# Optimization experiments

Hardware: AMD Instinct MI355X
Metric: run time of the kernel (lower is better)

## Reference

```python
import jax, jax.numpy as jnp
import numpy as np

N, H, B = 1048576, 128, 4096


def setup_inputs() -> dict:
    key = jax.random.key(0)
    ks = jax.random.split(key, 10)
    x = jax.random.normal(ks[0], (N, H), dtype=jnp.float32)
    # sorted segment ids with every segment nonempty (matches torch.bincount/split usage)
    batch = jnp.sort(jnp.concatenate([
        jnp.arange(B, dtype=jnp.int32),
        jax.random.randint(ks[1], (N - B,), 0, B, dtype=jnp.int32),
    ]))
    s = 1.0 / np.sqrt(H)
    u = lambda k, shp: jax.random.uniform(k, shp, jnp.float32, -s, s)
    return {
        'session_embedding': x,
        'batch': batch,
        'W1': u(ks[2], (H, H)), 'b1': u(ks[3], (H,)),
        'W2': u(ks[4], (H, H)), 'b2': u(ks[5], (H,)),
        'Wq': u(ks[6], (1, H)), 'bq': u(ks[7], (1,)),
        'W3': u(ks[8], (H, 2 * H)), 'b3': u(ks[9], (H,)),
    }


def reference(session_embedding, batch, W1, b1, W2, b2, Wq, bq, W3, b3):
    # index of the last node in each session (batch is sorted)
    last_idx = jax.ops.segment_max(jnp.arange(N, dtype=jnp.int32), batch, num_segments=B)  # [B]
    v_n = session_embedding[last_idx]                      # [B, H]
    v_n_rep = v_n[batch]                                   # [N, H] last-node broadcast per node
    # attention logits: q(sigmoid(W1 v_n + W2 v_i))
    gate = jax.nn.sigmoid(v_n_rep @ W1.T + b1 + session_embedding @ W2.T + b2)  # [N, H]
    alpha = gate @ Wq.T + bq                               # [N, 1]
    s_g = jax.ops.segment_sum(alpha * session_embedding, batch, num_segments=B)  # [B, H]
    s_h = jnp.concatenate([v_n, s_g], axis=1) @ W3.T + b3  # [B, H]
    return s_h
```

## Files before the change

kernel.cpp:

```cpp
#include <hip/hip_runtime.h>
#include <hip/hip_bf16.h>

#define N_NODES 1048576
#define H 128
#define B_SESS 4096
#define TILE 64

typedef __attribute__((ext_vector_type(8))) short bf16x8;
typedef __attribute__((ext_vector_type(4))) short bf16x4;
typedef __attribute__((ext_vector_type(4))) float f32x4;

__device__ inline short bc(float f) {
  return (short)__builtin_bit_cast(unsigned short, __float2bfloat16(f));
}

__global__ void k_prep(const int* __restrict__ batch, int* __restrict__ last_idx,
                       const float* __restrict__ W2, unsigned short* __restrict__ W2b,
                       float* __restrict__ s_g) {
  int i = blockIdx.x * 256 + threadIdx.x;
  if (i < N_NODES) {
    if (i == N_NODES - 1 || batch[i] != batch[i + 1]) last_idx[batch[i]] = i;
  }
  if (i < B_SESS * H) s_g[i] = 0.f;
  if (i < 4096) {
    float4 v = *reinterpret_cast<const float4*>(W2 + (size_t)i * 4);
    bf16x4 o;
    o[0] = bc(v.x); o[1] = bc(v.y); o[2] = bc(v.z); o[3] = bc(v.w);
    *reinterpret_cast<bf16x4*>(W2b + (size_t)i * 4) = o;
  }
}

__global__ void k_apre(const float* __restrict__ x, const int* __restrict__ last_idx,
                       const float* __restrict__ W1, const float* __restrict__ b1,
                       const float* __restrict__ b2, float* __restrict__ A_pre) {
  __shared__ float Wl[128][132];
  __shared__ float vn[8][128];
  int t = threadIdx.x;
  for (int i = 0; i < 16; ++i) {
    int e = (t + i * 256) * 4;
    int r = e >> 7, c = e & 127;
    float4 v = *reinterpret_cast<const float4*>(W1 + e);
    Wl[r][c] = v.x; Wl[r][c + 1] = v.y; Wl[r][c + 2] = v.z; Wl[r][c + 3] = v.w;
  }
  int b0 = blockIdx.x * 8;
  for (int i = t; i < 8 * 128; i += 256) {
    int s = i >> 7, c = i & 127;
    vn[s][c] = x[(size_t)last_idx[b0 + s] * H + c];
  }
  __syncthreads();
  int h = t & 127, si = t >> 7;
  float bias = b1[h] + b2[h];
  for (int s = si; s < 8; s += 2) {
    float acc = bias;
    #pragma unroll
    for (int k = 0; k < 128; k += 4) {
      float4 w = *reinterpret_cast<const float4*>(&Wl[h][k]);
      acc += vn[s][k] * w.x + vn[s][k + 1] * w.y + vn[s][k + 2] * w.z + vn[s][k + 3] * w.w;
    }
    A_pre[(size_t)(b0 + s) * H + h] = acc;
  }
}

__global__ __launch_bounds__(256, 4)
void k_main(const float* __restrict__ x, const int* __restrict__ batch,
            const unsigned short* __restrict__ W2b, const float* __restrict__ Wq,
            const float* __restrict__ bq, const float* __restrict__ A_pre,
            float* __restrict__ s_g) {
  __shared__ unsigned short Wl[128][136];
  __shared__ float alph[TILE];
  __shared__ int bseg[TILE + 1];
  int t = threadIdx.x;
  int node0 = blockIdx.x * TILE;
  int w = t >> 6, lane = t & 63, r = lane & 15, ks = lane >> 4;
  int myrow = w * 16 + r;

  float4 af[8];
  const float* xrow = x + (size_t)(node0 + myrow) * H;
  #pragma unroll
  for (int k = 0; k < 4; ++k) {
    af[2 * k]     = *reinterpret_cast<const float4*>(xrow + k * 32 + ks * 8);
    af[2 * k + 1] = *reinterpret_cast<const float4*>(xrow + k * 32 + ks * 8 + 4);
  }
  #pragma unroll
  for (int i = 0; i < 8; ++i) {
    int e = (t + i * 256) * 8;
    int rr = e >> 7, c = e & 127;
    *reinterpret_cast<bf16x8*>(&Wl[rr][c]) = *reinterpret_cast<const bf16x8*>(W2b + e);
  }
  if (t <= TILE) {
    int idx = node0 + t;
    bseg[t] = (idx < N_NODES) ? batch[idx] : -1;
  }
  __syncthreads();

  bf16x8 afr[4];
  #pragma unroll
  for (int k = 0; k < 4; ++k) {
    float4 lo = af[2 * k], hi = af[2 * k + 1];
    bf16x8 v;
    v[0] = bc(lo.x); v[1] = bc(lo.y); v[2] = bc(lo.z); v[3] = bc(lo.w);
    v[4] = bc(hi.x); v[5] = bc(hi.y); v[6] = bc(hi.z); v[7] = bc(hi.w);
    afr[k] = v;
  }

  f32x4 acc[8];
  #pragma unroll
  for (int nt = 0; nt < 8; ++nt) acc[nt] = (f32x4){0.f, 0.f, 0.f, 0.f};
  #pragma unroll
  for (int k = 0; k < 4; ++k) {
    #pragma unroll
    for (int nt = 0; nt < 8; ++nt) {
      bf16x8 b = *reinterpret_cast<const bf16x8*>(&Wl[nt * 16 + r][k * 32 + ks * 8]);
      acc[nt] = __builtin_amdgcn_mfma_f32_16x16x32_bf16(afr[k], b, acc[nt], 0, 0, 0);
    }
  }

  float bqv = bq[0];
  float pa[4];
  #pragma unroll
  for (int j = 0; j < 4; ++j) {
    const float* ap = A_pre + (size_t)bseg[w * 16 + ks * 4 + j] * H;
    float s = 0.f;
    #pragma unroll
    for (int nt = 0; nt < 8; ++nt) {
      float z = acc[nt][j] + ap[nt * 16 + r];
      float g = 1.0f / (1.0f + __expf(-z));
      s += g * Wq[nt * 16 + r];
    }
    s += __shfl_xor(s, 1);
    s += __shfl_xor(s, 2);
    s += __shfl_xor(s, 4);
    s += __shfl_xor(s, 8);
    pa[j] = s + bqv;
  }
  if (r == 0) {
    #pragma unroll
    for (int j = 0; j < 4; ++j) alph[w * 16 + ks * 4 + j] = pa[j];
  }
  __syncthreads();

  int h = t & 127, grp = t >> 7;
  int base = grp * 32;
  const float* xp = x + (size_t)(node0 + base) * H + h;
  float xv[32];
  #pragma unroll
  for (int n = 0; n < 32; ++n) xv[n] = xp[(size_t)n * H];
  float accum = 0.f;
  #pragma unroll
  for (int n = 0; n < 32; ++n) {
    int ln = base + n;
    accum += alph[ln] * xv[n];
    if (bseg[ln] != bseg[ln + 1]) {
      atomicAdd(&s_g[(size_t)bseg[ln] * H + h], accum);
      accum = 0.f;
    }
  }
  if (accum != 0.f) atomicAdd(&s_g[(size_t)bseg[base + 31] * H + h], accum);
}

__global__ void k_final(const float* __restrict__ x, const int* __restrict__ last_idx,
                        const float* __restrict__ s_g, const float* __restrict__ W3,
                        const float* __restrict__ b3, float* __restrict__ out) {
  __shared__ float Wl[128][132];
  __shared__ float vin[8][256];
  int t = threadIdx.x;
  int b0 = blockIdx.x * 8;
  for (int i = t; i < 8 * 256; i += 256) {
    int s = i >> 8, c = i & 255;
    float v;
    if (c < 128) v = x[(size_t)last_idx[b0 + s] * H + c];
    else         v = s_g[(size_t)(b0 + s) * H + (c - 128)];
    vin[s][c] = v;
  }
  int h = t & 127, si = t >> 7;
  float res[4];
  for (int half = 0; half < 2; ++half) {
    __syncthreads();
    for (int i = 0; i < 16; ++i) {
      int e = (t + i * 256) * 4;
      int r = e >> 7, c = e & 127;
      float4 v = *reinterpret_cast<const float4*>(W3 + (size_t)r * 256 + half * 128 + c);
      Wl[r][c] = v.x; Wl[r][c + 1] = v.y; Wl[r][c + 2] = v.z; Wl[r][c + 3] = v.w;
    }
    __syncthreads();
    #pragma unroll
    for (int sI = 0; sI < 4; ++sI) {
      int s = si + sI * 2;
      float acc = 0.f;
      #pragma unroll
      for (int k = 0; k < 128; k += 4) {
        float4 wv = *reinterpret_cast<const float4*>(&Wl[h][k]);
        acc += vin[s][half * 128 + k] * wv.x + vin[s][half * 128 + k + 1] * wv.y +
               vin[s][half * 128 + k + 2] * wv.z + vin[s][half * 128 + k + 3] * wv.w;
      }
      if (half == 0) res[sI] = acc;
      else out[(size_t)(b0 + s) * H + h] = res[sI] + acc + b3[h];
    }
  }
}

extern "C" void kernel_launch(void* const* d_in, const int* in_sizes, int n_in,
                              void* d_out, int out_size, void* d_ws, size_t ws_size,
                              hipStream_t stream) {
  const float* x     = (const float*)d_in[0];
  const int*   batch = (const int*)d_in[1];
  const float* W1    = (const float*)d_in[2];
  const float* b1    = (const float*)d_in[3];
  const float* W2    = (const float*)d_in[4];
  const float* b2    = (const float*)d_in[5];
  const float* Wq    = (const float*)d_in[6];
  const float* bq    = (const float*)d_in[7];
  const float* W3    = (const float*)d_in[8];
  const float* b3    = (const float*)d_in[9];
  float* out = (float*)d_out;

  char* ws = (char*)d_ws;
  int*            last_idx = (int*)ws;
  float*          A_pre    = (float*)(ws + 16384);
  float*          s_g      = (float*)(ws + 16384 + 2097152);
  unsigned short* W2b      = (unsigned short*)(ws + 16384 + 2 * 2097152);

  k_prep<<<N_NODES / 256, 256, 0, stream>>>(batch, last_idx, W2, W2b, s_g);
  k_apre<<<B_SESS / 8, 256, 0, stream>>>(x, last_idx, W1, b1, b2, A_pre);
  k_main<<<N_NODES / TILE, 256, 0, stream>>>(x, batch, W2b, Wq, bq, A_pre, s_g);
  k_final<<<B_SESS / 8, 256, 0, stream>>>(x, last_idx, s_g, W3, b3, out);
}
```

Measured before the change: 236.4 us.

## Halve W2 LDS footprint, stage A_pre and Wq in LDS, raise occupancy

The W2 tile is now loaded into LDS in two K-halves, so the shared array shrinks from 128x136 to 128x72 and launch bounds go from 4 to 5 blocks per CU. When a tile covers at most 16 segments, the needed A_pre rows are staged in LDS, and Wq is staged in LDS too, replacing scattered global loads in the sigmoid/alpha epilogue. The x loads for the segment-sum phase are issued before the alpha computation so their latency can overlap it. The costs are extra barriers for the two-phase W2 staging, more register pressure from holding W2 fragments and xv, and a fallback global path for tiles that span many segments.

```diff
diff --git a/kernel.cpp b/kernel.cpp
--- a/kernel.cpp
+++ b/kernel.cpp
@@ -61,14 +61,16 @@
   }
 }
 
-__global__ __launch_bounds__(256, 4)
+__global__ __launch_bounds__(256, 5)
 void k_main(const float* __restrict__ x, const int* __restrict__ batch,
             const unsigned short* __restrict__ W2b, const float* __restrict__ Wq,
             const float* __restrict__ bq, const float* __restrict__ A_pre,
             float* __restrict__ s_g) {
-  __shared__ unsigned short Wl[128][136];
+  __shared__ unsigned short Wl[128][72];
+  __shared__ float apre_s[16][128];
   __shared__ float alph[TILE];
-  __shared__ int bseg[TILE + 1];
+  __shared__ int bsegs[TILE + 1];
+  __shared__ float wqs[128];
   int t = threadIdx.x;
   int node0 = blockIdx.x * TILE;
   int w = t >> 6, lane = t & 63, r = lane & 15, ks = lane >> 4;
@@ -81,18 +83,32 @@
     af[2 * k]     = *reinterpret_cast<const float4*>(xrow + k * 32 + ks * 8);
     af[2 * k + 1] = *reinterpret_cast<const float4*>(xrow + k * 32 + ks * 8 + 4);
   }
-  #pragma unroll
-  for (int i = 0; i < 8; ++i) {
-    int e = (t + i * 256) * 8;
-    int rr = e >> 7, c = e & 127;
-    *reinterpret_cast<bf16x8*>(&Wl[rr][c]) = *reinterpret_cast<const bf16x8*>(W2b + e);
+  bf16x8 w0[4], w1[4];
+  #pragma unroll
+  for (int i = 0; i < 4; ++i) {
+    int u = t + i * 256, row = u >> 3, c = (u & 7) * 8;
+    w0[i] = *reinterpret_cast<const bf16x8*>(W2b + row * 128 + c);
+    w1[i] = *reinterpret_cast<const bf16x8*>(W2b + row * 128 + 64 + c);
+  }
+  int smin = batch[node0];
+  int smax = batch[node0 + TILE - 1];
+  int cnt = smax - smin + 1;
+  bool fast = (cnt <= 16);
+  if (fast) {
+    const float4* src = reinterpret_cast<const float4*>(A_pre + ((size_t)smin << 7));
+    float4* dst = reinterpret_cast<float4*>(&apre_s[0][0]);
+    for (int i = t; i < cnt * 32; i += 256) dst[i] = src[i];
   }
   if (t <= TILE) {
     int idx = node0 + t;
-    bseg[t] = (idx < N_NODES) ? batch[idx] : -1;
-  }
-  __syncthreads();
-
+    bsegs[t] = (idx < N_NODES) ? batch[idx] : -1;
+  }
+  if (t < 128) wqs[t] = Wq[t];
+  #pragma unroll
+  for (int i = 0; i < 4; ++i) {
+    int u = t + i * 256, row = u >> 3, c = (u & 7) * 8;
+    *reinterpret_cast<bf16x8*>(&Wl[row][c]) = w0[i];
+  }
   bf16x8 afr[4];
   #pragma unroll
   for (int k = 0; k < 4; ++k) {
@@ -102,42 +118,34 @@
     v[4] = bc(hi.x); v[5] = bc(hi.y); v[6] = bc(hi.z); v[7] = bc(hi.w);
     afr[k] = v;
   }
+  __syncthreads();
 
   f32x4 acc[8];
   #pragma unroll
   for (int nt = 0; nt < 8; ++nt) acc[nt] = (f32x4){0.f, 0.f, 0.f, 0.f};
   #pragma unroll
-  for (int k = 0; k < 4; ++k) {
+  for (int kg = 0; kg < 2; ++kg) {
     #pragma unroll
     for (int nt = 0; nt < 8; ++nt) {
-      bf16x8 b = *reinterpret_cast<const bf16x8*>(&Wl[nt * 16 + r][k * 32 + ks * 8]);
-      acc[nt] = __builtin_amdgcn_mfma_f32_16x16x32_bf16(afr[k], b, acc[nt], 0, 0, 0);
-    }
-  }
-
-  float bqv = bq[0];
-  float pa[4];
-  #pragma unroll
-  for (int j = 0; j < 4; ++j) {
-    const float* ap = A_pre + (size_t)bseg[w * 16 + ks * 4 + j] * H;
-    float s = 0.f;
+      bf16x8 b = *reinterpret_cast<const bf16x8*>(&Wl[nt * 16 + r][kg * 32 + ks * 8]);
+      acc[nt] = __builtin_amdgcn_mfma_f32_16x16x32_bf16(afr[kg], b, acc[nt], 0, 0, 0);
+    }
+  }
+  __syncthreads();
+  #pragma unroll
+  for (int i = 0; i < 4; ++i) {
+    int u = t + i * 256, row = u >> 3, c = (u & 7) * 8;
+    *reinterpret_cast<bf16x8*>(&Wl[row][c]) = w1[i];
+  }
+  __syncthreads();
+  #pragma unroll
+  for (int kg = 2; kg < 4; ++kg) {
     #pragma unroll
     for (int nt = 0; nt < 8; ++nt) {
-      float z = acc[nt][j] + ap[nt * 16 + r];
-      float g = 1.0f / (1.0f + __expf(-z));
-      s += g * Wq[nt * 16 + r];
-    }
-    s += __shfl_xor(s, 1);
-    s += __shfl_xor(s, 2);
-    s += __shfl_xor(s, 4);
-    s += __shfl_xor(s, 8);
-    pa[j] = s + bqv;
-  }
-  if (r == 0) {
-    #pragma unroll
-    for (int j = 0; j < 4; ++j) alph[w * 16 + ks * 4 + j] = pa[j];
-  }
-  __syncthreads();
+      bf16x8 b = *reinterpret_cast<const bf16x8*>(&Wl[nt * 16 + r][(kg - 2) * 32 + ks * 8]);
+      acc[nt] = __builtin_amdgcn_mfma_f32_16x16x32_bf16(afr[kg], b, acc[nt], 0, 0, 0);
+    }
+  }
 
   int h = t & 127, grp = t >> 7;
   int base = grp * 32;
@@ -145,17 +153,45 @@
   float xv[32];
   #pragma unroll
   for (int n = 0; n < 32; ++n) xv[n] = xp[(size_t)n * H];
+
+  float bqv = bq[0];
+  float pa[4];
+#define DO_ALPHA(GET) do {                                                   \
+    _Pragma("unroll")                                                        \
+    for (int j = 0; j < 4; ++j) {                                            \
+      int row = bsegs[w * 16 + ks * 4 + j];                                  \
+      float s = 0.f;                                                         \
+      _Pragma("unroll")                                                      \
+      for (int nt = 0; nt < 8; ++nt) {                                       \
+        int col = nt * 16 + r;                                               \
+        float z = acc[nt][j] + (GET);                                        \
+        float g = 1.0f / (1.0f + __expf(-z));                                \
+        s += g * wqs[col];                                                   \
+      }                                                                      \
+      s += __shfl_xor(s, 1); s += __shfl_xor(s, 2);                          \
+      s += __shfl_xor(s, 4); s += __shfl_xor(s, 8);                          \
+      pa[j] = s + bqv;                                                       \
+    } } while (0)
+  if (fast) DO_ALPHA(apre_s[row - smin][col]);
+  else      DO_ALPHA(A_pre[(size_t)row * H + col]);
+#undef DO_ALPHA
+  if (r == 0) {
+    #pragma unroll
+    for (int j = 0; j < 4; ++j) alph[w * 16 + ks * 4 + j] = pa[j];
+  }
+  __syncthreads();
+
   float accum = 0.f;
   #pragma unroll
   for (int n = 0; n < 32; ++n) {
     int ln = base + n;
     accum += alph[ln] * xv[n];
-    if (bseg[ln] != bseg[ln + 1]) {
-      atomicAdd(&s_g[(size_t)bseg[ln] * H + h], accum);
+    if (bsegs[ln] != bsegs[ln + 1]) {
+      atomicAdd(&s_g[(size_t)bsegs[ln] * H + h], accum);
       accum = 0.f;
     }
   }
-  if (accum != 0.f) atomicAdd(&s_g[(size_t)bseg[base + 31] * H + h], accum);
+  if (accum != 0.f) atomicAdd(&s_g[(size_t)bsegs[base + 31] * H + h], accum);
 }
 
 __global__ void k_final(const float* __restrict__ x, const int* __restrict__ last_idx,
```

Result: faster. 214.9 us (-9.1%).

## Reuse register-held x rows for segment reduction via wave shuffles, dropping second x read

Applied to the files above, without the earlier changes.

The main kernel now makes each wave own 16 nodes independently. It reduces alpha-weighted rows of x held in registers, which were already loaded as MFMA inputs, using cross-lane shuffles instead of rereading x from global memory through shared alpha and segment arrays. Segment ids are read once per lane and broadcast with shuffles, and Wq is hoisted into registers. This removes the second pass over x and a block barrier, but adds many shuffles and more atomics per segment, since partials are now flushed per 16-node wave.

```diff
diff --git a/kernel.cpp b/kernel.cpp
--- a/kernel.cpp
+++ b/kernel.cpp
@@ -4,7 +4,6 @@
 #define N_NODES 1048576
 #define H 128
 #define B_SESS 4096
-#define TILE 64
 
 typedef __attribute__((ext_vector_type(8))) short bf16x8;
 typedef __attribute__((ext_vector_type(4))) short bf16x4;
@@ -67,65 +66,70 @@
             const float* __restrict__ bq, const float* __restrict__ A_pre,
             float* __restrict__ s_g) {
   __shared__ unsigned short Wl[128][136];
-  __shared__ float alph[TILE];
-  __shared__ int bseg[TILE + 1];
   int t = threadIdx.x;
-  int node0 = blockIdx.x * TILE;
-  int w = t >> 6, lane = t & 63, r = lane & 15, ks = lane >> 4;
-  int myrow = w * 16 + r;
-
-  float4 af[8];
-  const float* xrow = x + (size_t)(node0 + myrow) * H;
-  #pragma unroll
-  for (int k = 0; k < 4; ++k) {
-    af[2 * k]     = *reinterpret_cast<const float4*>(xrow + k * 32 + ks * 8);
-    af[2 * k + 1] = *reinterpret_cast<const float4*>(xrow + k * 32 + ks * 8 + 4);
-  }
+  int lane = t & 63;
+  int r = lane & 15, ks = lane >> 4;
+  int node0 = (blockIdx.x * 4 + (t >> 6)) * 16;
+
   #pragma unroll
   for (int i = 0; i < 8; ++i) {
     int e = (t + i * 256) * 8;
     int rr = e >> 7, c = e & 127;
     *reinterpret_cast<bf16x8*>(&Wl[rr][c]) = *reinterpret_cast<const bf16x8*>(W2b + e);
   }
-  if (t <= TILE) {
-    int idx = node0 + t;
-    bseg[t] = (idx < N_NODES) ? batch[idx] : -1;
-  }
+
+  int myseg = batch[node0 + r];
+  int smin = __shfl(myseg, 0);
+  int smax = __shfl(myseg, 15);
+
+  const float* xrow = x + (size_t)(node0 + r) * H;
+  float4 af[8];
+  #pragma unroll
+  for (int k = 0; k < 4; ++k) {
+    af[2 * k]     = *reinterpret_cast<const float4*>(xrow + k * 32 + ks * 8);
+    af[2 * k + 1] = *reinterpret_cast<const float4*>(xrow + k * 32 + ks * 8 + 4);
+  }
+  const float* afp = reinterpret_cast<const float*>(af);
+
+  float wqv[8];
+  #pragma unroll
+  for (int nt = 0; nt < 8; ++nt) wqv[nt] = Wq[nt * 16 + r];
+  float bqv = bq[0];
+
+  bf16x8 afr[4];
+  #pragma unroll
+  for (int kg = 0; kg < 4; ++kg) {
+    bf16x8 v;
+    #pragma unroll
+    for (int c = 0; c < 8; ++c) v[c] = bc(afp[kg * 8 + c]);
+    afr[kg] = v;
+  }
+
   __syncthreads();
 
-  bf16x8 afr[4];
-  #pragma unroll
-  for (int k = 0; k < 4; ++k) {
-    float4 lo = af[2 * k], hi = af[2 * k + 1];
-    bf16x8 v;
-    v[0] = bc(lo.x); v[1] = bc(lo.y); v[2] = bc(lo.z); v[3] = bc(lo.w);
-    v[4] = bc(hi.x); v[5] = bc(hi.y); v[6] = bc(hi.z); v[7] = bc(hi.w);
-    afr[k] = v;
-  }
-
   f32x4 acc[8];
   #pragma unroll
   for (int nt = 0; nt < 8; ++nt) acc[nt] = (f32x4){0.f, 0.f, 0.f, 0.f};
   #pragma unroll
-  for (int k = 0; k < 4; ++k) {
+  for (int kg = 0; kg < 4; ++kg) {
     #pragma unroll
     for (int nt = 0; nt < 8; ++nt) {
-      bf16x8 b = *reinterpret_cast<const bf16x8*>(&Wl[nt * 16 + r][k * 32 + ks * 8]);
-      acc[nt] = __builtin_amdgcn_mfma_f32_16x16x32_bf16(afr[k], b, acc[nt], 0, 0, 0);
-    }
-  }
-
-  float bqv = bq[0];
+      bf16x8 b = *reinterpret_cast<const bf16x8*>(&Wl[nt * 16 + r][kg * 32 + ks * 8]);
+      acc[nt] = __builtin_amdgcn_mfma_f32_16x16x32_bf16(afr[kg], b, acc[nt], 0, 0, 0);
+    }
+  }
+
   float pa[4];
   #pragma unroll
   for (int j = 0; j < 4; ++j) {
-    const float* ap = A_pre + (size_t)bseg[w * 16 + ks * 4 + j] * H;
+    int segj = __shfl(myseg, (lane & 48) | (ks * 4 + j));
+    const float* ap = A_pre + ((size_t)segj << 7);
     float s = 0.f;
     #pragma unroll
     for (int nt = 0; nt < 8; ++nt) {
       float z = acc[nt][j] + ap[nt * 16 + r];
       float g = 1.0f / (1.0f + __expf(-z));
-      s += g * Wq[nt * 16 + r];
+      s += g * wqv[nt];
     }
     s += __shfl_xor(s, 1);
     s += __shfl_xor(s, 2);
@@ -133,29 +137,35 @@
     s += __shfl_xor(s, 8);
     pa[j] = s + bqv;
   }
-  if (r == 0) {
-    #pragma unroll
-    for (int j = 0; j < 4; ++j) alph[w * 16 + ks * 4 + j] = pa[j];
-  }
-  __syncthreads();
-
-  int h = t & 127, grp = t >> 7;
-  int base = grp * 32;
-  const float* xp = x + (size_t)(node0 + base) * H + h;
-  float xv[32];
-  #pragma unroll
-  for (int n = 0; n < 32; ++n) xv[n] = xp[(size_t)n * H];
-  float accum = 0.f;
-  #pragma unroll
-  for (int n = 0; n < 32; ++n) {
-    int ln = base + n;
-    accum += alph[ln] * xv[n];
-    if (bseg[ln] != bseg[ln + 1]) {
-      atomicAdd(&s_g[(size_t)bseg[ln] * H + h], accum);
-      accum = 0.f;
-    }
-  }
-  if (accum != 0.f) atomicAdd(&s_g[(size_t)bseg[base + 31] * H + h], accum);
+
+  int srcb = ((r >> 2) << 4) | r;
+  float g0 = __shfl(pa[0], srcb), g1 = __shfl(pa[1], srcb);
+  float g2 = __shfl(pa[2], srcb), g3 = __shfl(pa[3], srcb);
+  float a01 = (r & 1) ? g1 : g0;
+  float a23 = (r & 1) ? g3 : g2;
+  float ar  = (r & 2) ? a23 : a01;
+
+  for (int s = smin; s <= smax; ++s) {
+    float m = (myseg == s) ? ar : 0.f;
+    #pragma unroll
+    for (int kg = 0; kg < 4; ++kg) {
+      float v[8];
+      #pragma unroll
+      for (int c = 0; c < 8; ++c) v[c] = m * afp[kg * 8 + c];
+      #pragma unroll
+      for (int c = 0; c < 8; ++c) {
+        v[c] += __shfl_xor(v[c], 1);
+        v[c] += __shfl_xor(v[c], 2);
+        v[c] += __shfl_xor(v[c], 4);
+        v[c] += __shfl_xor(v[c], 8);
+      }
+      if (r == kg * 4) {
+        float* dst = s_g + ((size_t)s << 7) + kg * 32 + ks * 8;
+        #pragma unroll
+        for (int c = 0; c < 8; ++c) atomicAdd(dst + c, v[c]);
+      }
+    }
+  }
 }
 
 __global__ void k_final(const float* __restrict__ x, const int* __restrict__ last_idx,
@@ -222,6 +232,6 @@
 
   k_prep<<<N_NODES / 256, 256, 0, stream>>>(batch, last_idx, W2, W2b, s_g);
   k_apre<<<B_SESS / 8, 256, 0, stream>>>(x, last_idx, W1, b1, b2, A_pre);
-  k_main<<<N_NODES / TILE, 256, 0, stream>>>(x, batch, W2b, Wq, bq, A_pre, s_g);
+  k_main<<<N_NODES / 64, 256, 0, stream>>>(x, batch, W2b, Wq, bq, A_pre, s_g);
   k_final<<<B_SESS / 8, 256, 0, stream>>>(x, last_idx, s_g, W3, b3, out);
 }
```

New measurement: 418.3 us. +76.9%, slower.
